# Performance work log

Measured on AMD Instinct MI355X. Metric: run time of the kernel, lower is better.

## Reference

```python
import jax, jax.numpy as jnp
import numpy as np

# Model/config dims
U, B, D, H, R, S, M = 512, 16, 512, 8, 32, 16, 32
HD = D // H
Q = R + U + S          # query length
KV = M + R + U         # key/value length
PE = 2 * U - 1         # relative position embedding length (training mode)
NEG_INF = -1e8
SCALE = HD ** -0.5


def setup_inputs() -> dict:
    key = jax.random.key(0)
    ks = jax.random.split(key, 14)
    f = lambda k, shp: jax.random.normal(k, shp, dtype=jnp.float32)
    return {
        "utterance": f(ks[0], (U, B, D)),
        "lengths": jax.random.randint(ks[1], (B,), U // 2, U + 1),
        "right_context": f(ks[2], (R, B, D)),
        "summary": f(ks[3], (S, B, D)),
        "memory": f(ks[4], (M, B, D)),
        "attention_mask": jax.random.bernoulli(ks[5], 0.5, (Q, KV)),  # True = masked
        "pos_emb": f(ks[6], (PE, D)),
        "Wq": f(ks[7], (D, D)) * 0.02, "bq": jnp.zeros((D,), jnp.float32),
        "Wkv": f(ks[8], (2 * D, D)) * 0.02, "bkv": jnp.zeros((2 * D,), jnp.float32),
        "Wo": f(ks[9], (D, D)) * 0.02, "bo": jnp.zeros((D,), jnp.float32),
        "Wpos": f(ks[10], (D, D)) * 0.02,
        "pos_bias_u": f(ks[11], (H, HD)) * 0.02,
        "pos_bias_v": f(ks[12], (H, HD)) * 0.02,
    }


def _rel_shift(x):
    # x: (B, H, U, PE) -> (B, H, U, PE - U + 1); out[..., u, j] = x[..., u, (U-1) - u + j]
    b, h, u, pe = x.shape
    out_len = pe - (u - 1)
    idx = (u - 1) - jnp.arange(u)[:, None] + jnp.arange(out_len)[None, :]  # (U, out_len)
    return jnp.take_along_axis(x, idx[None, None], axis=3)


def reference(utterance, lengths, right_context, summary, memory, attention_mask,
              pos_emb, Wq, bq, Wkv, bkv, Wo, bo, Wpos, pos_bias_u, pos_bias_v):
    # Projections
    query = jnp.concatenate([right_context, utterance, summary]) @ Wq.T + bq      # (Q, B, D)
    kv = jnp.concatenate([memory, right_context, utterance]) @ Wkv.T + bkv        # (KV, B, 2D)
    key_t, val_t = jnp.split(kv, 2, axis=2)                                       # (KV, B, D) each

    rk = key_t.reshape(KV, B * H, HD).transpose(1, 0, 2)                          # (B*H, KV, HD)
    rv = val_t.reshape(KV, B * H, HD).transpose(1, 0, 2)
    q4 = query.reshape(Q, B, H, HD)

    # content term (matrix AC) with pos_bias_u
    qu = (q4 + pos_bias_u).reshape(Q, B * H, HD).transpose(1, 0, 2)               # (B*H, Q, HD)
    matrix_ac = jnp.einsum('nqd,nkd->nqk', qu, rk)                                # (B*H, Q, KV)

    # positional term (matrix BD) with pos_bias_v, only for utterance queries
    uv = (q4[R:R + U] + pos_bias_v).transpose(1, 2, 0, 3)                         # (B, H, U, HD)
    pos = (pos_emb @ Wpos.T).reshape(PE, H, HD).transpose(1, 0, 2)                # (H, PE, HD)
    bd = jnp.einsum('bhud,hpd->bhup', uv, pos)                                    # (B, H, U, PE)
    bd = _rel_shift(bd).reshape(B * H, U, -1)                                     # (B*H, U, U)
    matrix_bd = jnp.zeros_like(matrix_ac).at[:, R:R + U, M + R:].set(bd)

    w = (matrix_ac + matrix_bd) * SCALE
    w = jnp.where(attention_mask[None], NEG_INF, w)
    # padding mask (B > 1 branch): pad positions where kv index >= KV - U + lengths
    pad = jnp.arange(KV)[None, :] >= (KV - U + lengths)[:, None]                  # (B, KV)
    w = jnp.where(pad[:, None, None, :], NEG_INF, w.reshape(B, H, Q, KV)).reshape(B * H, Q, KV)

    probs = jax.nn.softmax(w, axis=-1)
    attn = jnp.einsum('nqk,nkd->nqd', probs, rv)                                  # (B*H, Q, HD)
    attn = attn.transpose(1, 0, 2).reshape(Q, B, D)
    outputs = attn @ Wo.T + bo

    out_right_context_utterance = outputs[:R + U]                                 # (R+U, B, D)
    out_memory = jnp.clip(outputs[R + U:], -10.0, 10.0)                           # (S, B, D), tanh_on_mem=False
    return out_right_context_utterance, out_memory, key_t, val_t
```

## Files before the change

### kernel.cpp

```cpp
#include <hip/hip_runtime.h>
#include <math.h>


#define NEG_INF_F (-100000000.0f)
#define SCALE_F   (0.125f)
#define LOG2E_F   (1.44269504f)

typedef short  short8 __attribute__((ext_vector_type(8)));
typedef float  f32x4  __attribute__((ext_vector_type(4)));
typedef unsigned short u16x4 __attribute__((ext_vector_type(4)));
typedef unsigned short u16x8 __attribute__((ext_vector_type(8)));

__device__ __forceinline__ unsigned short f2b(float f) {
    unsigned int u = __builtin_bit_cast(unsigned int, f);
    u = u + 0x7FFFu + ((u >> 16) & 1u);
    return (unsigned short)(u >> 16);
}
__device__ __forceinline__ float b2f(unsigned short h) {
    unsigned int u = ((unsigned int)h) << 16;
    return __builtin_bit_cast(float, u);
}

__device__ __forceinline__ float exp2_fast(float x) {
    float r;
    asm("v_exp_f32 %0, %1" : "=v"(r) : "v"(x));
    return r;
}

__device__ __forceinline__ void barrier_lg() {
    asm volatile("s_waitcnt lgkmcnt(0)\n\ts_barrier" ::: "memory");
}

__device__ __forceinline__ int swzK(int row, int colB) {
    return row * 64 + ((colB ^ ((row & 7) << 4)) >> 1);
}
__device__ __forceinline__ int swzS(int row, int colB) {
    return row * 576 + ((colB ^ ((row & 7) << 4)) >> 1);
}

__global__ __launch_bounds__(256) void conv9_kernel(
    const float* s0, const float* s1, const float* s2, const float* s3,
    const float* s4, const float* s5, const float* s6, const float* s7,
    const float* s8,
    unsigned short* d0, unsigned short* d1, unsigned short* d2,
    unsigned short* d3, unsigned short* d4, unsigned short* d5,
    unsigned short* d6, unsigned short* d7, unsigned short* d8,
    int n0, int n1, int n2, int n3, int n4, int n5, int n6, int n7, int n8,
    const unsigned int* __restrict__ mask, int nwords, int* __restrict__ flags)
{
    __shared__ int fF, fG;
    const int a = blockIdx.y;
    if (a == 9) {
        if (threadIdx.x == 0) { fF = 0; fG = 0; }
        __syncthreads();
        int lF = 0, lG = 0;
        for (int i = blockIdx.x * 256 + threadIdx.x; i < nwords; i += gridDim.x * 256) {
            unsigned int w = mask[i];
            if (w == 0x3F800000u)      lF = 1;
            else if (w > 1u)           lG = 1;
        }
        if (lF) atomicOr(&fF, 1);
        if (lG) atomicOr(&fG, 1);
        __syncthreads();
        if (threadIdx.x == 0) {
            if (fF) atomicOr(&flags[0], 1);
            if (fG) atomicOr(&flags[1], 1);
        }
        return;
    }
    const float* ss[9] = {s0, s1, s2, s3, s4, s5, s6, s7, s8};
    unsigned short* dd[9] = {d0, d1, d2, d3, d4, d5, d6, d7, d8};
    int nn[9] = {n0, n1, n2, n3, n4, n5, n6, n7, n8};
    const float* s = ss[a];
    unsigned short* d = dd[a];
    const int nq = nn[a] >> 2;
    for (int i = blockIdx.x * 256 + threadIdx.x; i < nq; i += gridDim.x * 256) {
        float4 v = *(const float4*)(s + (size_t)i * 4);
        u16x4 o = {f2b(v.x), f2b(v.y), f2b(v.z), f2b(v.w)};
        *(u16x4*)(d + (size_t)i * 4) = o;
    }
}

__global__ __launch_bounds__(256) void maskprep_kernel(
    const void* __restrict__ maskPtr, const int* __restrict__ flags,
    const int* __restrict__ lengths,
    unsigned short* __restrict__ maskBias, unsigned short* __restrict__ padBias)
{
    const int mode = flags[0] ? 2 : (flags[1] ? 1 : 0);
    const unsigned short NB = f2b(NEG_INF_F);
    for (int i = blockIdx.x * 256 + threadIdx.x; i < 560 * 576; i += gridDim.x * 256) {
        bool m;
        if (mode == 1)      m = ((const unsigned char*)maskPtr)[i] != 0;
        else if (mode == 2) m = ((const float*)maskPtr)[i] != 0.f;
        else                m = ((const int*)maskPtr)[i] != 0;
        maskBias[i] = m ? NB : (unsigned short)0;
    }
    for (int i = blockIdx.x * 256 + threadIdx.x; i < 16 * 576; i += gridDim.x * 256) {
        int b = i / 576, k = i - b * 576;
        padBias[i] = (k >= 64 + lengths[b]) ? NB : (unsigned short)0;
    }
}

struct GemmJob {
    const unsigned short *a0, *a1, *a2;
    int rb1, rb2, Mrows;
    const unsigned short *Wt;
    const float *bias;
    float *out0, *out1;
    unsigned short *auxU, *auxV;
    const float *pbu, *pbv;
    int mode, clampStart;
    int nBlocks;
    int base;
};

__global__ __launch_bounds__(256) void gemm_mfma3(GemmJob J0, GemmJob J1, GemmJob J2)
{
    __shared__ __attribute__((aligned(16))) unsigned short As[128 * 64];
    __shared__ __attribute__((aligned(16))) unsigned short Ws[128 * 64];

    const int cpx = gridDim.x >> 3;
    const int bid = (blockIdx.x & 7) * cpx + (blockIdx.x >> 3);

    GemmJob J;
    if (bid >= J2.base)      J = J2;
    else if (bid >= J1.base) J = J1;
    else                     J = J0;
    const int rel = bid - J.base;
    const int bn = (rel % J.nBlocks) * 128;
    const int bm = (rel / J.nBlocks) * 128;

    const int tid = threadIdx.x;
    const int w = tid >> 6, lane = tid & 63;
    const int l15 = lane & 15, l4 = lane >> 4;
    const int wm = (w & 1) * 64, wn = (w >> 1) * 64;

    const int lrow  = lane >> 3;
    const int lslot = lane & 7;
    const int swzS16 = (lslot ^ lrow) * 8;

    const unsigned short* srcA[4];
    const unsigned short* srcW[4];
    #pragma unroll
    for (int c = 0; c < 4; ++c) {
        const int row = w * 32 + c * 8 + lrow;
        const int r = bm + row;
        const unsigned short* s;
        if (r < J.rb1)      s = J.a0 + (size_t)r * 512;
        else if (r < J.rb2) s = J.a1 + (size_t)(r - J.rb1) * 512;
        else                s = J.a2 + (size_t)(r - J.rb2) * 512;
        srcA[c] = s + swzS16;
        srcW[c] = J.Wt + (size_t)(bn + row) * 512 + swzS16;
    }

    f32x4 acc[4][4];
    #pragma unroll
    for (int i = 0; i < 4; ++i)
        #pragma unroll
        for (int j = 0; j < 4; ++j) acc[i][j] = (f32x4){0.f, 0.f, 0.f, 0.f};

    #define GFRAG(arr, row, kk) \
        (*(const short8*)&arr[(row) * 64 + ((((kk) * 4 + l4) ^ ((row) & 7)) * 8)])

    for (int kt = 0; kt < 8; ++kt) {
        __syncthreads();
        #pragma unroll
        for (int c = 0; c < 4; ++c) {
            __builtin_amdgcn_global_load_lds(
                (const __attribute__((address_space(1))) unsigned int*)(srcA[c] + kt * 64),
                (__attribute__((address_space(3))) unsigned int*)&As[(w * 32 + c * 8) * 64],
                16, 0, 0);
            __builtin_amdgcn_global_load_lds(
                (const __attribute__((address_space(1))) unsigned int*)(srcW[c] + kt * 64),
                (__attribute__((address_space(3))) unsigned int*)&Ws[(w * 32 + c * 8) * 64],
                16, 0, 0);
        }
        __syncthreads();

        short8 bfr[4][2];
        #pragma unroll
        for (int t = 0; t < 4; ++t) {
            const int r = wn + t * 16 + l15;
            bfr[t][0] = GFRAG(Ws, r, 0);
            bfr[t][1] = GFRAG(Ws, r, 1);
        }
        #pragma unroll
        for (int tm = 0; tm < 4; ++tm) {
            const int r = wm + tm * 16 + l15;
            const short8 a0f = GFRAG(As, r, 0);
            const short8 a1f = GFRAG(As, r, 1);
            #pragma unroll
            for (int tn = 0; tn < 4; ++tn) {
                acc[tm][tn] = __builtin_amdgcn_mfma_f32_16x16x32_bf16(
                    a0f, bfr[tn][0], acc[tm][tn], 0, 0, 0);
                acc[tm][tn] = __builtin_amdgcn_mfma_f32_16x16x32_bf16(
                    a1f, bfr[tn][1], acc[tm][tn], 0, 0, 0);
            }
        }
    }
    #undef GFRAG

    #pragma unroll
    for (int tm = 0; tm < 4; ++tm) {
        #pragma unroll
        for (int tn = 0; tn < 4; ++tn) {
            const int col = bn + wn + tn * 16 + l15;
            const float bv = J.bias ? J.bias[col] : 0.f;
            #pragma unroll
            for (int rr = 0; rr < 4; ++rr) {
                const int row = bm + wm + tm * 16 + l4 * 4 + rr;
                if (row >= J.Mrows) continue;
                float v = acc[tm][tn][rr] + bv;
                if (J.mode == 0) {
                    if (row >= J.clampStart) v = fminf(fmaxf(v, -10.f), 10.f);
                    J.out0[(size_t)row * 512 + col] = v;
                } else if (J.mode == 1) {
                    int bb = row & 15, kv = row >> 4;
                    if (col < 512) {
                        J.out0[(size_t)row * 512 + col] = v;
                        int hh = col >> 6, hd = col & 63;
                        J.auxU[(((size_t)(bb * 8 + hh)) * 576 + kv) * 64 + hd] = f2b(v);
                    } else {
                        J.out1[(size_t)row * 512 + (col - 512)] = v;
                        int cc = col - 512, hh = cc >> 6, hd = cc & 63;
                        J.auxV[(((size_t)(bb * 8 + hh)) * 64 + hd) * 576 + kv] = f2b(v);
                    }
                } else if (J.mode == 2) {
                    int q = row >> 4, bb = row & 15, hh = col >> 6, hd = col & 63;
                    size_t base = (((size_t)(bb * 8 + hh)) * 576 + q) * 64 + hd;
                    J.auxU[base] = f2b((v + J.pbu[col]) * (SCALE_F * LOG2E_F));
                    J.auxV[base] = f2b((v + J.pbv[col]) * (SCALE_F * LOG2E_F));
                } else {
                    int hh = col >> 6, hd = col & 63;
                    J.auxU[((size_t)hh * 1023 + row) * 64 + hd] = f2b(v);
                }
            }
        }
    }
}

__global__ __launch_bounds__(256) void attn_mfma_kernel(
    const unsigned short* __restrict__ Qu_g,
    const unsigned short* __restrict__ Qv_g,
    const unsigned short* __restrict__ K_g,
    const unsigned short* __restrict__ VT_g,
    const unsigned short* __restrict__ P_g,
    const unsigned short* __restrict__ maskBias,
    const unsigned short* __restrict__ padBias,
    unsigned short* __restrict__ attnT)
{
    __shared__ __attribute__((aligned(16))) unsigned short sc[32 * 576];
    __shared__ __attribute__((aligned(16))) unsigned short stg[2 * 4096];
    __shared__ float rowv[32];

    const int bid = blockIdx.y * 18 + blockIdx.x;
    const int workid = (bid & 7) * 288 + (bid >> 3);
    const int n = workid / 18;
    const int qt = workid - n * 18;

    const int b = n >> 3, h = n & 7;
    const int q0 = qt * 32;
    const int tid = threadIdx.x;
    const int w = tid >> 6, lane = tid & 63;
    const int l15 = lane & 15, l4 = lane >> 4;
    const int mT = (w >> 1) * 16;
    const int c0 = (w & 1) * 32;
    const int t0base = 16 - mT + c0;
    const bool hasBand = (qt >= 1 && qt <= 16);
    const int pbq = 512 - q0;

    const unsigned short* Kn  = K_g  + (size_t)n * 576 * 64;
    const unsigned short* VTn = VT_g + (size_t)n * 64 * 576;
    const unsigned short* Ph  = P_g  + (size_t)h * 1023 * 64;

    const int srow  = tid >> 3;
    const int sIdx  = (tid & 7) * 8;
    const int scolB = sIdx * 2;

    {
        u16x8 a = *(const u16x8*)&Kn[(size_t)srow * 64 + sIdx];
        u16x8 c = *(const u16x8*)&Kn[(size_t)(srow + 32) * 64 + sIdx];
        *(u16x8*)&stg[swzK(srow, scolB)] = a;
        *(u16x8*)&stg[swzK(srow + 32, scolB)] = c;
    }

    short8 quf[2], qvf[2];
    {
        size_t rb = ((size_t)n * 576 + q0 + mT + l15) * 64;
        quf[0] = *(const short8*)&Qu_g[rb + l4 * 8];
        quf[1] = *(const short8*)&Qu_g[rb + 32 + l4 * 8];
        qvf[0] = *(const short8*)&Qv_g[rb + l4 * 8];
        qvf[1] = *(const short8*)&Qv_g[rb + 32 + l4 * 8];
    }

    int cur = 0;
    for (int kt = 0; kt < 9; ++kt) {
        u16x8 kna, knb;
        if (kt < 8) {
            kna = *(const u16x8*)&Kn[(size_t)((kt + 1) * 64 + srow) * 64 + sIdx];
            knb = *(const u16x8*)&Kn[(size_t)((kt + 1) * 64 + srow + 32) * 64 + sIdx];
        }
        const bool doBand = hasBand && (kt >= 1);
        short8 bnd00, bnd01, bnd10, bnd11, bnd20, bnd21;
        if (doBand) {
            const int pbase = pbq + (kt - 1) * 64 + t0base + l15;
            int p0 = pbase;       p0 = p0 < 0 ? 0 : (p0 > 1022 ? 1022 : p0);
            int p1 = pbase + 16;  p1 = p1 < 0 ? 0 : (p1 > 1022 ? 1022 : p1);
            int p2 = pbase + 32;  p2 = p2 < 0 ? 0 : (p2 > 1022 ? 1022 : p2);
            bnd00 = *(const short8*)&Ph[(size_t)p0 * 64 + l4 * 8];
            bnd01 = *(const short8*)&Ph[(size_t)p0 * 64 + 32 + l4 * 8];
            bnd10 = *(const short8*)&Ph[(size_t)p1 * 64 + l4 * 8];
            bnd11 = *(const short8*)&Ph[(size_t)p1 * 64 + 32 + l4 * 8];
            bnd20 = *(const short8*)&Ph[(size_t)p2 * 64 + l4 * 8];
            bnd21 = *(const short8*)&Ph[(size_t)p2 * 64 + 32 + l4 * 8];
        }
        barrier_lg();
        unsigned short* buf = stg + cur * 4096;
        __builtin_amdgcn_s_setprio(1);
        #pragma unroll
        for (int s = 0; s < 2; ++s) {
            const int n0 = c0 + s * 16;
            f32x4 acc = {0.f, 0.f, 0.f, 0.f};
            short8 b0 = *(const short8*)&buf[swzK(n0 + l15, l4 * 16)];
            short8 b1 = *(const short8*)&buf[swzK(n0 + l15, 64 + l4 * 16)];
            acc = __builtin_amdgcn_mfma_f32_16x16x32_bf16(quf[0], b0, acc, 0, 0, 0);
            acc = __builtin_amdgcn_mfma_f32_16x16x32_bf16(quf[1], b1, acc, 0, 0, 0);
            const int col = kt * 64 + n0 + l15;
            #pragma unroll
            for (int r = 0; r < 4; ++r)
                sc[swzS(mT + l4 * 4 + r, col * 2)] = f2b(acc[r]);
        }
        __builtin_amdgcn_s_setprio(0);
        if (doBand) {
            #pragma unroll
            for (int s = 0; s < 3; ++s) {
                short8 ba = (s == 0) ? bnd00 : ((s == 1) ? bnd10 : bnd20);
                short8 bb = (s == 0) ? bnd01 : ((s == 1) ? bnd11 : bnd21);
                f32x4 acc = {0.f, 0.f, 0.f, 0.f};
                acc = __builtin_amdgcn_mfma_f32_16x16x32_bf16(qvf[0], ba, acc, 0, 0, 0);
                acc = __builtin_amdgcn_mfma_f32_16x16x32_bf16(qvf[1], bb, acc, 0, 0, 0);
                const int tl = t0base + s * 16 + l15;
                #pragma unroll
                for (int r = 0; r < 4; ++r) {
                    const int du = mT + l4 * 4 + r;
                    const int dj = tl - 31 + du;
                    if (dj >= c0 && dj < c0 + 32) {
                        const int ix = swzS(du, (kt * 64 + dj) * 2);
                        sc[ix] = f2b(b2f(sc[ix]) + acc[r]);
                    }
                }
            }
        }
        if (kt < 8) {
            unsigned short* nb = stg + (cur ^ 1) * 4096;
            *(u16x8*)&nb[swzK(srow, scolB)] = kna;
            *(u16x8*)&nb[swzK(srow + 32, scolB)] = knb;
        }
        cur ^= 1;
    }

    u16x8 va = *(const u16x8*)&VTn[(size_t)srow * 576 + sIdx];
    u16x8 vb = *(const u16x8*)&VTn[(size_t)(srow + 32) * 576 + sIdx];
    barrier_lg();

    {
        const int row = tid >> 3, seg = tid & 7;
        const int q = q0 + row;
        const int qc = q < 560 ? q : 559;
        const unsigned short* mb  = maskBias + (size_t)qc * 576 + seg * 72;
        const unsigned short* pbb = padBias + (size_t)b * 576 + seg * 72;
        float mx = -3.0e38f;
        #pragma unroll
        for (int ci = 0; ci < 9; ++ci) {
            u16x8 sv = *(const u16x8*)&sc[swzS(row, seg * 144 + ci * 16)];
            u16x8 mv = *(const u16x8*)&mb[ci * 8];
            u16x8 pv = *(const u16x8*)&pbb[ci * 8];
            #pragma unroll
            for (int j = 0; j < 8; ++j)
                mx = fmaxf(mx, b2f(sv[j]) + b2f(mv[j]) + b2f(pv[j]));
        }
        mx = fmaxf(mx, __shfl_xor(mx, 1));
        mx = fmaxf(mx, __shfl_xor(mx, 2));
        mx = fmaxf(mx, __shfl_xor(mx, 4));
        float lsum = 0.f;
        #pragma unroll
        for (int ci = 0; ci < 9; ++ci) {
            const int ix = swzS(row, seg * 144 + ci * 16);
            u16x8 sv = *(const u16x8*)&sc[ix];
            u16x8 mv = *(const u16x8*)&mb[ci * 8];
            u16x8 pv = *(const u16x8*)&pbb[ci * 8];
            u16x8 ev;
            #pragma unroll
            for (int j = 0; j < 8; ++j) {
                float e = exp2_fast(b2f(sv[j]) + b2f(mv[j]) + b2f(pv[j]) - mx);
                ev[j] = f2b(e); lsum += e;
            }
            *(u16x8*)&sc[ix] = ev;
        }
        lsum += __shfl_xor(lsum, 1);
        lsum += __shfl_xor(lsum, 2);
        lsum += __shfl_xor(lsum, 4);
        if (seg == 0) rowv[row] = 1.f / lsum;
    }
    *(u16x8*)&stg[swzK(srow, scolB)] = va;
    *(u16x8*)&stg[swzK(srow + 32, scolB)] = vb;

    f32x4 oacc0 = {0.f, 0.f, 0.f, 0.f}, oacc1 = {0.f, 0.f, 0.f, 0.f};
    cur = 0;
    for (int kt = 0; kt < 9; ++kt) {
        u16x8 vna, vnb;
        if (kt < 8) {
            vna = *(const u16x8*)&VTn[(size_t)srow * 576 + (kt + 1) * 64 + sIdx];
            vnb = *(const u16x8*)&VTn[(size_t)(srow + 32) * 576 + (kt + 1) * 64 + sIdx];
        }
        barrier_lg();
        unsigned short* buf = stg + cur * 4096;
        short8 af0 = *(const short8*)&sc[swzS(mT + l15, kt * 128 + l4 * 16)];
        short8 af1 = *(const short8*)&sc[swzS(mT + l15, kt * 128 + 64 + l4 * 16)];
        __builtin_amdgcn_s_setprio(1);
        {
            short8 b00 = *(const short8*)&buf[swzK(c0 + l15, l4 * 16)];
            short8 b01 = *(const short8*)&buf[swzK(c0 + l15, 64 + l4 * 16)];
            short8 b10 = *(const short8*)&buf[swzK(c0 + 16 + l15, l4 * 16)];
            short8 b11 = *(const short8*)&buf[swzK(c0 + 16 + l15, 64 + l4 * 16)];
            oacc0 = __builtin_amdgcn_mfma_f32_16x16x32_bf16(af0, b00, oacc0, 0, 0, 0);
            oacc0 = __builtin_amdgcn_mfma_f32_16x16x32_bf16(af1, b01, oacc0, 0, 0, 0);
            oacc1 = __builtin_amdgcn_mfma_f32_16x16x32_bf16(af0, b10, oacc1, 0, 0, 0);
            oacc1 = __builtin_amdgcn_mfma_f32_16x16x32_bf16(af1, b11, oacc1, 0, 0, 0);
        }
        __builtin_amdgcn_s_setprio(0);
        if (kt < 8) {
            unsigned short* nb = stg + (cur ^ 1) * 4096;
            *(u16x8*)&nb[swzK(srow, scolB)] = vna;
            *(u16x8*)&nb[swzK(srow + 32, scolB)] = vnb;
        }
        cur ^= 1;
    }

    #pragma unroll
    for (int s = 0; s < 2; ++s) {
        const f32x4 oa = s ? oacc1 : oacc0;
        const int n0 = c0 + s * 16;
        #pragma unroll
        for (int r = 0; r < 4; ++r) {
            const int row = mT + l4 * 4 + r, q = q0 + row;
            if (q < 560)
                attnT[((size_t)q * 16 + b) * 512 + h * 64 + n0 + l15] =
                    f2b(oa[r] * rowv[row]);
        }
    }
}

extern "C" void kernel_launch(void* const* d_in, const int* in_sizes, int n_in,
                              void* d_out, int out_size, void* d_ws, size_t ws_size,
                              hipStream_t stream) {
    const float* utt     = (const float*)d_in[0];
    const int*   lengths = (const int*)d_in[1];
    const float* rc      = (const float*)d_in[2];
    const float* summ    = (const float*)d_in[3];
    const float* mem     = (const float*)d_in[4];
    const void*  mask    = d_in[5];
    const float* pos_emb = (const float*)d_in[6];
    const float* Wq      = (const float*)d_in[7];
    const float* bq      = (const float*)d_in[8];
    const float* Wkv     = (const float*)d_in[9];
    const float* bkv     = (const float*)d_in[10];
    const float* Wo      = (const float*)d_in[11];
    const float* bo      = (const float*)d_in[12];
    const float* Wpos    = (const float*)d_in[13];
    const float* pbu     = (const float*)d_in[14];
    const float* pbv     = (const float*)d_in[15];

    float* out = (float*)d_out;
    float* out0   = out;
    float* keyOut = out + 4587520;
    float* valOut = out + 9306112;

    int* flags = (int*)d_ws;
    unsigned short* U = (unsigned short*)d_ws + 64;
    unsigned short* utt_bf  = U;
    unsigned short* rc_bf   = utt_bf  + 4194304;
    unsigned short* summ_bf = rc_bf   + 262144;
    unsigned short* mem_bf  = summ_bf + 131072;
    unsigned short* pose_bf = mem_bf  + 262144;
    unsigned short* wq_bf   = pose_bf + 523776;
    unsigned short* wkv_bf  = wq_bf   + 262144;
    unsigned short* wo_bf   = wkv_bf  + 524288;
    unsigned short* wpos_bf = wo_bf   + 262144;
    unsigned short* Qu_bf   = wpos_bf + 262144;
    unsigned short* Qv_bf   = Qu_bf   + 4718592;
    unsigned short* K_bf    = Qv_bf   + 4718592;
    unsigned short* VT_bf   = K_bf    + 4718592;
    unsigned short* posW_bf = VT_bf   + 4718592;
    unsigned short* attnT_bf= posW_bf + 523776;
    unsigned short* maskB   = attnT_bf + 4587520;
    unsigned short* padB    = maskB + 322560;

    (void)hipMemsetAsync(flags, 0, 2 * sizeof(int), stream);

    conv9_kernel<<<dim3(1024, 10), 256, 0, stream>>>(
        utt, rc, summ, mem, pos_emb, Wq, Wkv, Wo, Wpos,
        utt_bf, rc_bf, summ_bf, mem_bf, pose_bf, wq_bf, wkv_bf, wo_bf, wpos_bf,
        4194304, 262144, 131072, 262144, 523776, 262144, 524288, 262144, 262144,
        (const unsigned int*)mask, (560 * 576) / 4, flags);

    maskprep_kernel<<<315, 256, 0, stream>>>(mask, flags, lengths, maskB, padB);

    GemmJob jq;
    jq.a0 = rc_bf; jq.a1 = utt_bf; jq.a2 = summ_bf;
    jq.rb1 = 512; jq.rb2 = 8704; jq.Mrows = 8960;
    jq.Wt = wq_bf; jq.bias = bq;
    jq.out0 = nullptr; jq.out1 = nullptr;
    jq.auxU = Qu_bf; jq.auxV = Qv_bf;
    jq.pbu = pbu; jq.pbv = pbv;
    jq.mode = 2; jq.clampStart = 0; jq.nBlocks = 4; jq.base = 0;

    GemmJob jkv;
    jkv.a0 = mem_bf; jkv.a1 = rc_bf; jkv.a2 = utt_bf;
    jkv.rb1 = 512; jkv.rb2 = 1024; jkv.Mrows = 9216;
    jkv.Wt = wkv_bf; jkv.bias = bkv;
    jkv.out0 = keyOut; jkv.out1 = valOut;
    jkv.auxU = K_bf; jkv.auxV = VT_bf;
    jkv.pbu = nullptr; jkv.pbv = nullptr;
    jkv.mode = 1; jkv.clampStart = 0; jkv.nBlocks = 8; jkv.base = 280;

    GemmJob jp;
    jp.a0 = pose_bf; jp.a1 = pose_bf; jp.a2 = pose_bf;
    jp.rb1 = 1 << 30; jp.rb2 = 1 << 30; jp.Mrows = 1023;
    jp.Wt = wpos_bf; jp.bias = nullptr;
    jp.out0 = nullptr; jp.out1 = nullptr;
    jp.auxU = posW_bf; jp.auxV = nullptr;
    jp.pbu = nullptr; jp.pbv = nullptr;
    jp.mode = 3; jp.clampStart = 0; jp.nBlocks = 4; jp.base = 856;

    gemm_mfma3<<<888, 256, 0, stream>>>(jq, jkv, jp);

    attn_mfma_kernel<<<dim3(18, 128), 256, 0, stream>>>(
        Qu_bf, Qv_bf, K_bf, VT_bf, posW_bf, maskB, padB, attnT_bf);

    GemmJob jo;
    jo.a0 = attnT_bf; jo.a1 = attnT_bf; jo.a2 = attnT_bf;
    jo.rb1 = 1 << 30; jo.rb2 = 1 << 30; jo.Mrows = 8960;
    jo.Wt = wo_bf; jo.bias = bo;
    jo.out0 = out0; jo.out1 = nullptr;
    jo.auxU = nullptr; jo.auxV = nullptr;
    jo.pbu = nullptr; jo.pbv = nullptr;
    jo.mode = 0; jo.clampStart = 8704; jo.nBlocks = 4; jo.base = 0;

    GemmJob jdummy = jo;
    jdummy.base = 1 << 30;

    gemm_mfma3<<<280, 256, 0, stream>>>(jo, jdummy, jdummy);
}
```

Baseline: 295.1 us.

## Fuse mask and padding preparation into attention softmax, drop XCD block remap

Removes the separate maskprep kernel and has the attention kernel read the raw attention mask (in whatever dtype the flags say) and the lengths directly. It packs them into per-thread bitmasks that select NEG_INF during the softmax max and exp passes, which drops the bias-tensor writes and reads plus one launch. Separately, the GEMM kernel no longer remaps block IDs across the 8 XCDs, which may change L2 locality. The raw mask read is wider per element for int/float masks and uses scalar loads, and 128 blocks re-read each mask row.

```diff
diff --git a/kernel.cpp b/kernel.cpp
--- a/kernel.cpp
+++ b/kernel.cpp
@@ -81,26 +81,6 @@
     }
 }
 
-__global__ __launch_bounds__(256) void maskprep_kernel(
-    const void* __restrict__ maskPtr, const int* __restrict__ flags,
-    const int* __restrict__ lengths,
-    unsigned short* __restrict__ maskBias, unsigned short* __restrict__ padBias)
-{
-    const int mode = flags[0] ? 2 : (flags[1] ? 1 : 0);
-    const unsigned short NB = f2b(NEG_INF_F);
-    for (int i = blockIdx.x * 256 + threadIdx.x; i < 560 * 576; i += gridDim.x * 256) {
-        bool m;
-        if (mode == 1)      m = ((const unsigned char*)maskPtr)[i] != 0;
-        else if (mode == 2) m = ((const float*)maskPtr)[i] != 0.f;
-        else                m = ((const int*)maskPtr)[i] != 0;
-        maskBias[i] = m ? NB : (unsigned short)0;
-    }
-    for (int i = blockIdx.x * 256 + threadIdx.x; i < 16 * 576; i += gridDim.x * 256) {
-        int b = i / 576, k = i - b * 576;
-        padBias[i] = (k >= 64 + lengths[b]) ? NB : (unsigned short)0;
-    }
-}
-
 struct GemmJob {
     const unsigned short *a0, *a1, *a2;
     int rb1, rb2, Mrows;
@@ -119,8 +99,7 @@
     __shared__ __attribute__((aligned(16))) unsigned short As[128 * 64];
     __shared__ __attribute__((aligned(16))) unsigned short Ws[128 * 64];
 
-    const int cpx = gridDim.x >> 3;
-    const int bid = (blockIdx.x & 7) * cpx + (blockIdx.x >> 3);
+    const int bid = blockIdx.x;
 
     GemmJob J;
     if (bid >= J2.base)      J = J2;
@@ -245,8 +224,9 @@
     const unsigned short* __restrict__ K_g,
     const unsigned short* __restrict__ VT_g,
     const unsigned short* __restrict__ P_g,
-    const unsigned short* __restrict__ maskBias,
-    const unsigned short* __restrict__ padBias,
+    const void* __restrict__ maskPtr,
+    const int* __restrict__ flags,
+    const int* __restrict__ lengths,
     unsigned short* __restrict__ attnT)
 {
     __shared__ __attribute__((aligned(16))) unsigned short sc[32 * 576];
@@ -367,17 +347,47 @@
         const int row = tid >> 3, seg = tid & 7;
         const int q = q0 + row;
         const int qc = q < 560 ? q : 559;
-        const unsigned short* mb  = maskBias + (size_t)qc * 576 + seg * 72;
-        const unsigned short* pbb = padBias + (size_t)b * 576 + seg * 72;
+        const int kbase = seg * 72;
+        const int mode = flags[0] ? 2 : (flags[1] ? 1 : 0);
+        const int padk = 64 + lengths[b];
+
+        unsigned int mw0 = 0, mw1 = 0, mw2 = 0;
+        #pragma unroll
+        for (int ci = 0; ci < 9; ++ci) {
+            const int k0 = kbase + ci * 8;
+            unsigned int bits = 0;
+            if (mode == 2) {
+                const float* mp = (const float*)maskPtr + (size_t)qc * 576 + k0;
+                #pragma unroll
+                for (int j = 0; j < 8; ++j) bits |= (mp[j] != 0.f ? 1u : 0u) << j;
+            } else if (mode == 1) {
+                const unsigned char* mp = (const unsigned char*)maskPtr + (size_t)qc * 576 + k0;
+                #pragma unroll
+                for (int j = 0; j < 8; ++j) bits |= (mp[j] != 0 ? 1u : 0u) << j;
+            } else {
+                const int* mp = (const int*)maskPtr + (size_t)qc * 576 + k0;
+                #pragma unroll
+                for (int j = 0; j < 8; ++j) bits |= (mp[j] != 0 ? 1u : 0u) << j;
+            }
+            #pragma unroll
+            for (int j = 0; j < 8; ++j)
+                if (k0 + j >= padk) bits |= 1u << j;
+            if (ci < 4)      mw0 |= bits << (ci * 8);
+            else if (ci < 8) mw1 |= bits << ((ci - 4) * 8);
+            else             mw2 |= bits;
+        }
+
         float mx = -3.0e38f;
         #pragma unroll
         for (int ci = 0; ci < 9; ++ci) {
-            u16x8 sv = *(const u16x8*)&sc[swzS(row, seg * 144 + ci * 16)];
-            u16x8 mv = *(const u16x8*)&mb[ci * 8];
-            u16x8 pv = *(const u16x8*)&pbb[ci * 8];
-            #pragma unroll
-            for (int j = 0; j < 8; ++j)
-                mx = fmaxf(mx, b2f(sv[j]) + b2f(mv[j]) + b2f(pv[j]));
+            u16x8 sv = *(const u16x8*)&sc[swzS(row, kbase * 2 + ci * 16)];
+            const unsigned int bits =
+                (ci < 4) ? (mw0 >> (ci * 8)) : ((ci < 8) ? (mw1 >> ((ci - 4) * 8)) : mw2);
+            #pragma unroll
+            for (int j = 0; j < 8; ++j) {
+                float v = (bits & (1u << j)) ? NEG_INF_F : b2f(sv[j]);
+                mx = fmaxf(mx, v);
+            }
         }
         mx = fmaxf(mx, __shfl_xor(mx, 1));
         mx = fmaxf(mx, __shfl_xor(mx, 2));
@@ -385,14 +395,15 @@
         float lsum = 0.f;
         #pragma unroll
         for (int ci = 0; ci < 9; ++ci) {
-            const int ix = swzS(row, seg * 144 + ci * 16);
+            const int ix = swzS(row, kbase * 2 + ci * 16);
             u16x8 sv = *(const u16x8*)&sc[ix];
-            u16x8 mv = *(const u16x8*)&mb[ci * 8];
-            u16x8 pv = *(const u16x8*)&pbb[ci * 8];
+            const unsigned int bits =
+                (ci < 4) ? (mw0 >> (ci * 8)) : ((ci < 8) ? (mw1 >> ((ci - 4) * 8)) : mw2);
             u16x8 ev;
             #pragma unroll
             for (int j = 0; j < 8; ++j) {
-                float e = exp2_fast(b2f(sv[j]) + b2f(mv[j]) + b2f(pv[j]) - mx);
+                float v = (bits & (1u << j)) ? NEG_INF_F : b2f(sv[j]);
+                float e = exp2_fast(v - mx);
                 ev[j] = f2b(e); lsum += e;
             }
             *(u16x8*)&sc[ix] = ev;
@@ -493,8 +504,6 @@
     unsigned short* VT_bf   = K_bf    + 4718592;
     unsigned short* posW_bf = VT_bf   + 4718592;
     unsigned short* attnT_bf= posW_bf + 523776;
-    unsigned short* maskB   = attnT_bf + 4587520;
-    unsigned short* padB    = maskB + 322560;
 
     (void)hipMemsetAsync(flags, 0, 2 * sizeof(int), stream);
 
@@ -503,8 +512,6 @@
         utt_bf, rc_bf, summ_bf, mem_bf, pose_bf, wq_bf, wkv_bf, wo_bf, wpos_bf,
         4194304, 262144, 131072, 262144, 523776, 262144, 524288, 262144, 262144,
         (const unsigned int*)mask, (560 * 576) / 4, flags);
-
-    maskprep_kernel<<<315, 256, 0, stream>>>(mask, flags, lengths, maskB, padB);
 
     GemmJob jq;
     jq.a0 = rc_bf; jq.a1 = utt_bf; jq.a2 = summ_bf;
@@ -536,7 +543,7 @@
     gemm_mfma3<<<888, 256, 0, stream>>>(jq, jkv, jp);
 
     attn_mfma_kernel<<<dim3(18, 128), 256, 0, stream>>>(
-        Qu_bf, Qv_bf, K_bf, VT_bf, posW_bf, maskB, padB, attnT_bf);
+        Qu_bf, Qv_bf, K_bf, VT_bf, posW_bf, mask, flags, lengths, attnT_bf);
 
     GemmJob jo;
     jo.a0 = attnT_bf; jo.a1 = attnT_bf; jo.a2 = attnT_bf;
```

New measurement: 308.6 us. +4.6%, slower.
